# Optimization experiments

Measured on AMD Instinct MI355X. Metric: run time of the kernel, lower is better.

Reference implementation:

```python
import jax, jax.numpy as jnp
import numpy as np

N_NODES = 50000
N_EDGES = 800000
NFEAT = 256
NHID = 128
NCLASS = 40
NLAYERS = 3


def setup_inputs() -> dict:
    key = jax.random.key(0)
    ks = jax.random.split(key, 8)
    x = jax.random.normal(ks[0], (N_NODES, NFEAT), dtype=jnp.float32)
    edge_src = jax.random.randint(ks[1], (N_EDGES,), 0, N_NODES, dtype=jnp.int32)
    edge_dst = jax.random.randint(ks[2], (N_EDGES,), 0, N_NODES, dtype=jnp.int32)
    # Kaiming-ish scaled params
    W_in = jax.random.normal(ks[3], (NFEAT, NHID), dtype=jnp.float32) / np.sqrt(NFEAT)
    b_in = jnp.zeros((NHID,), dtype=jnp.float32)
    W_mlps = jax.random.normal(ks[4], (NLAYERS, NHID, NHID), dtype=jnp.float32) / np.sqrt(NHID)
    b_mlps = jnp.zeros((NLAYERS, NHID), dtype=jnp.float32)
    W_out = jax.random.normal(ks[5], (NHID, NCLASS), dtype=jnp.float32) / np.sqrt(NHID)
    b_out = jnp.zeros((NCLASS,), dtype=jnp.float32)
    return {"x": x, "edge_src": edge_src, "edge_dst": edge_dst,
            "W_in": W_in, "b_in": b_in, "W_mlps": W_mlps, "b_mlps": b_mlps,
            "W_out": W_out, "b_out": b_out}


def reference(x, edge_src, edge_dst, W_in, b_in, W_mlps, b_mlps, W_out, b_out):
    # Dropout is identity in eval mode (training=False).
    n = x.shape[0]
    h = jax.nn.relu(x @ W_in + b_in)                       # [N, H]
    for i in range(NLAYERS):
        # GINConv with eps=0: h' = h + sum_{(s->d) in E} h[s] scattered to d
        agg = jax.ops.segment_sum(h[edge_src], edge_dst, num_segments=n)
        h = jax.nn.relu((h + agg) @ W_mlps[i] + b_mlps[i])  # [N, H]
    logits = h @ W_out + b_out                              # [N, C]
    return jax.nn.log_softmax(logits, axis=1)
```

## Files before the change

kernel.cpp:

```cpp
#include <hip/hip_runtime.h>
#include <math.h>

#define NHID 128
#define NFEAT 256
#define NCLASS 40

typedef __bf16 bf16x8 __attribute__((ext_vector_type(8)));
typedef __bf16 bf16x4 __attribute__((ext_vector_type(4)));
typedef float floatx4 __attribute__((ext_vector_type(4)));


__global__ __launch_bounds__(256) void bucket_hist(const int* __restrict__ edst,
                                                   int* __restrict__ bucket_counts,
                                                   int E, int nbuck) {
    __shared__ int lh[256];
    int tid = threadIdx.x;
    lh[tid] = 0;
    __syncthreads();
    int base = blockIdx.x * 4096;
#pragma unroll
    for (int k = 0; k < 16; ++k) {
        int e = base + k * 256 + tid;
        if (e < E) atomicAdd(&lh[edst[e] >> 8], 1);
    }
    __syncthreads();
    if (tid < nbuck && lh[tid]) atomicAdd(&bucket_counts[tid], lh[tid]);
}

__global__ __launch_bounds__(256) void bucket_scan(const int* __restrict__ counts,
                                                   int* __restrict__ start,
                                                   int* __restrict__ cursor,
                                                   int* __restrict__ row_ptr,
                                                   int nbuck, int E, int N) {
    __shared__ int lds[256];
    int tid = threadIdx.x;
    int v = (tid < nbuck) ? counts[tid] : 0;
    lds[tid] = v;
    __syncthreads();
    for (int off = 1; off < 256; off <<= 1) {
        int t = (tid >= off) ? lds[tid - off] : 0;
        __syncthreads();
        lds[tid] += t;
        __syncthreads();
    }
    int excl = lds[tid] - v;
    if (tid < nbuck) { start[tid] = excl; cursor[tid] = excl; }
    if (tid == 0) { start[nbuck] = E; row_ptr[N] = E; }
}

__global__ __launch_bounds__(256) void bucket_scatter(const int* __restrict__ esrc,
                                                      const int* __restrict__ edst,
                                                      int* __restrict__ cursor,
                                                      unsigned int* __restrict__ bdata,
                                                      int E, int nbuck) {
    __shared__ int lh[256];
    __shared__ int lbase[256];
    int tid = threadIdx.x;
    lh[tid] = 0;
    __syncthreads();
    int base = blockIdx.x * 4096;
    unsigned int recs[16];
    short bks[16];
    short lofs[16];
#pragma unroll
    for (int k = 0; k < 16; ++k) {
        int e = base + k * 256 + tid;
        bks[k] = -1;
        if (e < E) {
            int d = edst[e];
            int s = esrc[e];
            int b = d >> 8;
            recs[k] = ((unsigned int)(d & 255) << 16) | (unsigned int)s;
            bks[k] = (short)b;
            lofs[k] = (short)atomicAdd(&lh[b], 1);
        }
    }
    __syncthreads();
    if (tid < nbuck && lh[tid]) lbase[tid] = atomicAdd(&cursor[tid], lh[tid]);
    __syncthreads();
#pragma unroll
    for (int k = 0; k < 16; ++k) {
        if (bks[k] >= 0) bdata[lbase[bks[k]] + lofs[k]] = recs[k];
    }
}

__global__ __launch_bounds__(256) void bucket_finalize(const unsigned int* __restrict__ bdata,
                                                       const int* __restrict__ start,
                                                       int* __restrict__ row_ptr,
                                                       int* __restrict__ srcs,
                                                       int N) {
    __shared__ int hist[256];
    __shared__ int cur[256];
    int b = blockIdx.x;
    int tid = threadIdx.x;
    int s0 = start[b];
    int cnt = start[b + 1] - s0;
    hist[tid] = 0;
    __syncthreads();
    for (int i = tid; i < cnt; i += 256) atomicAdd(&hist[bdata[s0 + i] >> 16], 1);
    __syncthreads();
    int v0 = hist[tid];
    __syncthreads();
    for (int off = 1; off < 256; off <<= 1) {
        int t = (tid >= off) ? hist[tid - off] : 0;
        __syncthreads();
        hist[tid] += t;
        __syncthreads();
    }
    int excl = hist[tid] - v0;
    cur[tid] = excl;
    int node = b * 256 + tid;
    if (node < N) row_ptr[node] = s0 + excl;
    __syncthreads();
    for (int i = tid; i < cnt; i += 256) {
        unsigned int r = bdata[s0 + i];
        int p = atomicAdd(&cur[r >> 16], 1);
        srcs[s0 + p] = (int)(r & 0xffffu);
    }
}

template <int K>
__global__ __launch_bounds__(256) void transpose_split(const float* __restrict__ src,
                                                       __bf16* __restrict__ dhi,
                                                       __bf16* __restrict__ dlo, int total) {
    int i = blockIdx.x * 256 + threadIdx.x;
    if (i >= total) return;
    int per = 128 * K;
    int l = i / per;
    int r = i - l * per;
    int n = r / K;
    int k = r - n * K;
    float v = src[(size_t)l * per + (size_t)k * 128 + n];
    __bf16 hi = (__bf16)v;
    dhi[i] = hi;
    dlo[i] = (__bf16)(v - (float)hi);
}

__global__ __launch_bounds__(256) void aggregate_fused(const __bf16* __restrict__ hhi,
                                                       const __bf16* __restrict__ hlo,
                                                       const int* __restrict__ row_ptr,
                                                       const int* __restrict__ srcs,
                                                       __bf16* __restrict__ ohi,
                                                       __bf16* __restrict__ olo, int N) {
    int tid = threadIdx.x;
    int node = blockIdx.x * 4 + (tid >> 6);
    if (node >= N) return;
    int lane = tid & 63;
    int g = lane >> 4;
    int c = lane & 15;
    int beg = row_ptr[node];
    int end = row_ptr[node + 1];
    const bf16x8* hv = (const bf16x8*)hhi;

    float a[8], b2[8];
#pragma unroll
    for (int j = 0; j < 8; ++j) { a[j] = 0.f; b2[j] = 0.f; }

    int i = beg;
    for (; i + 8 <= end; i += 8) {
        int s0 = srcs[i + g];
        int s1 = srcs[i + 4 + g];
        bf16x8 v0 = hv[(size_t)s0 * 16 + c];
        bf16x8 v1 = hv[(size_t)s1 * 16 + c];
#pragma unroll
        for (int j = 0; j < 8; ++j) { a[j] += (float)v0[j]; b2[j] += (float)v1[j]; }
    }
    for (; i < end; i += 4) {
        if (i + g < end) {
            int s = srcs[i + g];
            bf16x8 v = hv[(size_t)s * 16 + c];
#pragma unroll
            for (int j = 0; j < 8; ++j) a[j] += (float)v[j];
        }
    }
#pragma unroll
    for (int j = 0; j < 8; ++j) a[j] += b2[j];
#pragma unroll
    for (int j = 0; j < 8; ++j) a[j] += __shfl_xor(a[j], 16);
#pragma unroll
    for (int j = 0; j < 8; ++j) a[j] += __shfl_xor(a[j], 32);

    if (g == 0) {
        bf16x8 sh = ((const bf16x8*)hhi)[(size_t)node * 16 + c];
        bf16x8 sl = ((const bf16x8*)hlo)[(size_t)node * 16 + c];
        bf16x8 whi, wlo;
#pragma unroll
        for (int j = 0; j < 8; ++j) {
            float v = a[j] + (float)sh[j] + (float)sl[j];
            __bf16 h = (__bf16)v;
            whi[j] = h;
            wlo[j] = (__bf16)(v - (float)h);
        }
        ((bf16x8*)ohi)[(size_t)node * 16 + c] = whi;
        ((bf16x8*)olo)[(size_t)node * 16 + c] = wlo;
    }
}

template <int MODE>
__global__ __launch_bounds__(256) void gemm_mfma(
    const float* __restrict__ Af, const __bf16* __restrict__ Ahi,
    const __bf16* __restrict__ Alo,
    const __bf16* __restrict__ Wthi, const __bf16* __restrict__ Wtlo,
    const float* __restrict__ bias, __bf16* __restrict__ Ohi,
    __bf16* __restrict__ Olo, int M, int K) {
    __shared__ __align__(16) char smem[49152];
    __bf16* sAhi = (__bf16*)smem;
    __bf16* sAlo = (__bf16*)(smem + 8192);
    __bf16* sWhi = (__bf16*)(smem + 16384);
    __bf16* sWlo = (__bf16*)(smem + 32768);

    int tid = threadIdx.x;
    int row0 = blockIdx.x * 64;
    int wave = tid >> 6;
    int l = tid & 63;
    int m16 = l & 15;
    int q = l >> 4;
    int axor = m16 & 7;
    int arow = wave * 16 + m16;

    floatx4 acc[8];
#pragma unroll
    for (int t = 0; t < 8; ++t) acc[t] = (floatx4){0.f, 0.f, 0.f, 0.f};

    for (int k0 = 0; k0 < K; k0 += 64) {
#pragma unroll
        for (int it = 0; it < 2; ++it) {
            int lin = it * 2048 + tid * 8;
            int row = lin >> 6, k = lin & 63;
            int g = min(row0 + row, M - 1);
            int off = row * 64 + (((k >> 3) ^ (row & 7)) << 3);
            if (MODE == 0) {
                float4 v0 = *(const float4*)&Af[(size_t)g * K + k0 + k];
                float4 v1 = *(const float4*)&Af[(size_t)g * K + k0 + k + 4];
                float s[8] = {v0.x, v0.y, v0.z, v0.w, v1.x, v1.y, v1.z, v1.w};
                bf16x8 shi, slo;
#pragma unroll
                for (int j = 0; j < 8; ++j) {
                    __bf16 h = (__bf16)s[j];
                    shi[j] = h;
                    slo[j] = (__bf16)(s[j] - (float)h);
                }
                *(bf16x8*)(sAhi + off) = shi;
                *(bf16x8*)(sAlo + off) = slo;
            } else {
                *(bf16x8*)(sAhi + off) = *(const bf16x8*)&Ahi[(size_t)g * 128 + k0 + k];
                *(bf16x8*)(sAlo + off) = *(const bf16x8*)&Alo[(size_t)g * 128 + k0 + k];
            }
        }
#pragma unroll
        for (int it = 0; it < 4; ++it) {
            int lin = it * 2048 + tid * 8;
            int n = lin >> 6, kk = lin & 63;
            int off = n * 64 + (((kk >> 3) ^ (n & 7)) << 3);
            *(bf16x8*)(sWhi + off) = *(const bf16x8*)&Wthi[(size_t)n * K + k0 + kk];
            *(bf16x8*)(sWlo + off) = *(const bf16x8*)&Wtlo[(size_t)n * K + k0 + kk];
        }
        __syncthreads();

#pragma unroll
        for (int s = 0; s < 2; ++s) {
            int sw = (((s * 4 + q) ^ axor) << 3);
            bf16x8 ahi = *(bf16x8*)(sAhi + arow * 64 + sw);
            bf16x8 alo = *(bf16x8*)(sAlo + arow * 64 + sw);
#pragma unroll
            for (int t = 0; t < 8; ++t) {
                int n = t * 16 + m16;
                bf16x8 bhi = *(bf16x8*)(sWhi + n * 64 + sw);
                bf16x8 blo = *(bf16x8*)(sWlo + n * 64 + sw);
                acc[t] = __builtin_amdgcn_mfma_f32_16x16x32_bf16(ahi, bhi, acc[t], 0, 0, 0);
                acc[t] = __builtin_amdgcn_mfma_f32_16x16x32_bf16(alo, bhi, acc[t], 0, 0, 0);
                acc[t] = __builtin_amdgcn_mfma_f32_16x16x32_bf16(ahi, blo, acc[t], 0, 0, 0);
            }
        }
        __syncthreads();
    }

    float* eps = (float*)(smem + 16384);
#pragma unroll
    for (int t = 0; t < 8; ++t) {
        int col = t * 16 + m16;
        float bb = bias[col];
#pragma unroll
        for (int i = 0; i < 4; ++i) {
            int row = wave * 16 + q * 4 + i;
            eps[row * 128 + col] = fmaxf(acc[t][i] + bb, 0.f);
        }
    }
    __syncthreads();
#pragma unroll
    for (int it = 0; it < 8; ++it) {
        int lin = it * 1024 + tid * 4;
        int row = lin >> 7, col = lin & 127;
        int g = row0 + row;
        if (g < M) {
            float4 v = *(float4*)(eps + lin);
            bf16x4 hi, lo;
            float vv[4] = {v.x, v.y, v.z, v.w};
#pragma unroll
            for (int j = 0; j < 4; ++j) {
                __bf16 h = (__bf16)vv[j];
                hi[j] = h;
                lo[j] = (__bf16)(vv[j] - (float)h);
            }
            *(bf16x4*)&Ohi[(size_t)g * 128 + col] = hi;
            *(bf16x4*)&Olo[(size_t)g * 128 + col] = lo;
        }
    }
}

__global__ __launch_bounds__(256) void out_logsoftmax(const __bf16* __restrict__ hhi,
                                                      const __bf16* __restrict__ hlo,
                                                      const float* __restrict__ Wout,
                                                      const float* __restrict__ bout,
                                                      float* __restrict__ out, int M) {
    __shared__ float sW[128 * NCLASS];
    __shared__ float sb[NCLASS];
    __shared__ float sH[32 * 132];
    int tid = threadIdx.x;
    for (int i = tid; i < 128 * NCLASS; i += 256) sW[i] = Wout[i];
    if (tid < NCLASS) sb[tid] = bout[tid];
    int row0 = blockIdx.x * 32;
#pragma unroll
    for (int it = 0; it < 4; ++it) {
        int i = tid * 4 + it * 1024;
        int r = i >> 7, k = i & 127;
        int rr = min(row0 + r, M - 1);
        uint2 uh = *(const uint2*)&hhi[(size_t)rr * 128 + k];
        uint2 ul = *(const uint2*)&hlo[(size_t)rr * 128 + k];
        sH[r * 132 + k + 0] = __uint_as_float(uh.x << 16) + __uint_as_float(ul.x << 16);
        sH[r * 132 + k + 1] = __uint_as_float(uh.x & 0xffff0000u) + __uint_as_float(ul.x & 0xffff0000u);
        sH[r * 132 + k + 2] = __uint_as_float(uh.y << 16) + __uint_as_float(ul.y << 16);
        sH[r * 132 + k + 3] = __uint_as_float(uh.y & 0xffff0000u) + __uint_as_float(ul.y & 0xffff0000u);
    }
    __syncthreads();

    int r = tid >> 3;
    int cg = tid & 7;
    float z[5];
#pragma unroll
    for (int j = 0; j < 5; ++j) z[j] = sb[cg * 5 + j];
    for (int k = 0; k < 128; ++k) {
        float a = sH[r * 132 + k];
#pragma unroll
        for (int j = 0; j < 5; ++j) z[j] += a * sW[k * NCLASS + cg * 5 + j];
    }
    float m = z[0];
#pragma unroll
    for (int j = 1; j < 5; ++j) m = fmaxf(m, z[j]);
    for (int off = 1; off < 8; off <<= 1) m = fmaxf(m, __shfl_xor(m, off));
    float s = 0.f;
#pragma unroll
    for (int j = 0; j < 5; ++j) s += expf(z[j] - m);
    for (int off = 1; off < 8; off <<= 1) s += __shfl_xor(s, off);
    float lse = m + logf(s);
    int row = row0 + r;
    if (row < M) {
#pragma unroll
        for (int j = 0; j < 5; ++j) out[(size_t)row * NCLASS + cg * 5 + j] = z[j] - lse;
    }
}

extern "C" void kernel_launch(void* const* d_in, const int* in_sizes, int n_in,
                              void* d_out, int out_size, void* d_ws, size_t ws_size,
                              hipStream_t stream) {
    const float* x      = (const float*)d_in[0];
    const int*   esrc   = (const int*)d_in[1];
    const int*   edst   = (const int*)d_in[2];
    const float* W_in   = (const float*)d_in[3];
    const float* b_in   = (const float*)d_in[4];
    const float* W_mlps = (const float*)d_in[5];
    const float* b_mlps = (const float*)d_in[6];
    const float* W_out  = (const float*)d_in[7];
    const float* b_out  = (const float*)d_in[8];
    float* out = (float*)d_out;

    int N = in_sizes[0] / NFEAT;
    int E = in_sizes[1];
    int nbuck = (N + 255) >> 8;

    char* ws = (char*)d_ws;
    size_t hb = (((size_t)N * NHID * sizeof(__bf16)) + 255) & ~(size_t)255;
    __bf16* h_hi_a = (__bf16*)ws;
    __bf16* h_lo_a = (__bf16*)(ws + hb);
    __bf16* h_hi_b = (__bf16*)(ws + 2 * hb);
    __bf16* h_lo_b = (__bf16*)(ws + 3 * hb);
    __bf16* sum_hi = (__bf16*)(ws + 4 * hb);
    __bf16* sum_lo = (__bf16*)(ws + 5 * hb);
    unsigned int* bdata = (unsigned int*)(ws + 4 * hb);
    char* ip = ws + 6 * hb;
    int* row_ptr = (int*)ip;  ip += (((size_t)(N + 1) * 4) + 255) & ~(size_t)255;
    int* srcs    = (int*)ip;  ip += (((size_t)E * 4) + 255) & ~(size_t)255;
    int* bucket_counts = (int*)ip;  ip += 1024;
    int* bucket_start  = (int*)ip;  ip += 1024;
    int* bucket_cursor = (int*)ip;  ip += 1024;
    __bf16* Wt_in_hi   = (__bf16*)ip;  ip += 128 * NFEAT * 2;
    __bf16* Wt_in_lo   = (__bf16*)ip;  ip += 128 * NFEAT * 2;
    __bf16* Wt_mlps_hi = (__bf16*)ip;  ip += 3 * 128 * NHID * 2;
    __bf16* Wt_mlps_lo = (__bf16*)ip;  ip += 3 * 128 * NHID * 2;

    int eb4 = (E + 4095) / 4096;

    hipMemsetAsync(bucket_counts, 0, 1024, stream);
    bucket_hist<<<eb4, 256, 0, stream>>>(edst, bucket_counts, E, nbuck);
    bucket_scan<<<1, 256, 0, stream>>>(bucket_counts, bucket_start, bucket_cursor,
                                       row_ptr, nbuck, E, N);
    bucket_scatter<<<eb4, 256, 0, stream>>>(esrc, edst, bucket_cursor, bdata, E, nbuck);
    bucket_finalize<<<nbuck, 256, 0, stream>>>(bdata, bucket_start, row_ptr, srcs, N);

    transpose_split<NFEAT><<<(128 * NFEAT + 255) / 256, 256, 0, stream>>>(
        W_in, Wt_in_hi, Wt_in_lo, 128 * NFEAT);
    transpose_split<NHID><<<(3 * 128 * NHID + 255) / 256, 256, 0, stream>>>(
        W_mlps, Wt_mlps_hi, Wt_mlps_lo, 3 * 128 * NHID);

    int gb = (N + 63) / 64;
    gemm_mfma<0><<<gb, 256, 0, stream>>>(x, (const __bf16*)nullptr, (const __bf16*)nullptr,
                                         Wt_in_hi, Wt_in_lo, b_in, h_hi_a, h_lo_a, N, NFEAT);

    __bf16* cur_hi = h_hi_a; __bf16* cur_lo = h_lo_a;
    __bf16* nxt_hi = h_hi_b; __bf16* nxt_lo = h_lo_b;
    for (int i = 0; i < 3; ++i) {
        aggregate_fused<<<(N + 3) / 4, 256, 0, stream>>>(cur_hi, cur_lo, row_ptr, srcs,
                                                         sum_hi, sum_lo, N);
        gemm_mfma<1><<<gb, 256, 0, stream>>>(
            (const float*)nullptr, sum_hi, sum_lo,
            Wt_mlps_hi + (size_t)i * 128 * NHID, Wt_mlps_lo + (size_t)i * 128 * NHID,
            b_mlps + (size_t)i * NHID, nxt_hi, nxt_lo, N, NHID);
        __bf16* t;
        t = cur_hi; cur_hi = nxt_hi; nxt_hi = t;
        t = cur_lo; cur_lo = nxt_lo; nxt_lo = t;
    }

    out_logsoftmax<<<(N + 31) / 32, 256, 0, stream>>>(cur_hi, cur_lo, W_out, b_out, out, N);
}
```

Baseline: 336.9 us.

## Fuse GIN aggregation with per-layer MLP GEMM and merge weight transposes

Each GIN layer now runs as one kernel: a block of 32 nodes gathers neighbour sums into shared memory as a bf16 hi/lo split, then runs the 128x128 MFMA GEMM with bias and ReLU directly on that tile. The intermediate sum buffers and their global round trip go away, along with one launch per layer. The two weight transpose kernels are merged into one launch. In exchange, weights are read straight from global memory per wave rather than staged in LDS, and each wave gathers 8 nodes serially, which may lower memory-level parallelism in the gather.

Result: slower. 353.9 us (+5.0%).

```diff
diff --git a/kernel.cpp b/kernel.cpp
--- a/kernel.cpp
+++ b/kernel.cpp
@@ -8,7 +8,6 @@
 typedef __bf16 bf16x8 __attribute__((ext_vector_type(8)));
 typedef __bf16 bf16x4 __attribute__((ext_vector_type(4)));
 typedef float floatx4 __attribute__((ext_vector_type(4)));
-
 
 __global__ __launch_bounds__(256) void bucket_hist(const int* __restrict__ edst,
                                                    int* __restrict__ bucket_counts,
@@ -119,87 +118,33 @@
     }
 }
 
-template <int K>
-__global__ __launch_bounds__(256) void transpose_split(const float* __restrict__ src,
-                                                       __bf16* __restrict__ dhi,
-                                                       __bf16* __restrict__ dlo, int total) {
+__global__ __launch_bounds__(256) void transpose_split_all(
+    const float* __restrict__ W_in, const float* __restrict__ W_mlps,
+    __bf16* __restrict__ in_hi, __bf16* __restrict__ in_lo,
+    __bf16* __restrict__ ml_hi, __bf16* __restrict__ ml_lo) {
     int i = blockIdx.x * 256 + threadIdx.x;
-    if (i >= total) return;
-    int per = 128 * K;
-    int l = i / per;
-    int r = i - l * per;
-    int n = r / K;
-    int k = r - n * K;
-    float v = src[(size_t)l * per + (size_t)k * 128 + n];
-    __bf16 hi = (__bf16)v;
-    dhi[i] = hi;
-    dlo[i] = (__bf16)(v - (float)hi);
-}
-
-__global__ __launch_bounds__(256) void aggregate_fused(const __bf16* __restrict__ hhi,
-                                                       const __bf16* __restrict__ hlo,
-                                                       const int* __restrict__ row_ptr,
-                                                       const int* __restrict__ srcs,
-                                                       __bf16* __restrict__ ohi,
-                                                       __bf16* __restrict__ olo, int N) {
-    int tid = threadIdx.x;
-    int node = blockIdx.x * 4 + (tid >> 6);
-    if (node >= N) return;
-    int lane = tid & 63;
-    int g = lane >> 4;
-    int c = lane & 15;
-    int beg = row_ptr[node];
-    int end = row_ptr[node + 1];
-    const bf16x8* hv = (const bf16x8*)hhi;
-
-    float a[8], b2[8];
-#pragma unroll
-    for (int j = 0; j < 8; ++j) { a[j] = 0.f; b2[j] = 0.f; }
-
-    int i = beg;
-    for (; i + 8 <= end; i += 8) {
-        int s0 = srcs[i + g];
-        int s1 = srcs[i + 4 + g];
-        bf16x8 v0 = hv[(size_t)s0 * 16 + c];
-        bf16x8 v1 = hv[(size_t)s1 * 16 + c];
-#pragma unroll
-        for (int j = 0; j < 8; ++j) { a[j] += (float)v0[j]; b2[j] += (float)v1[j]; }
-    }
-    for (; i < end; i += 4) {
-        if (i + g < end) {
-            int s = srcs[i + g];
-            bf16x8 v = hv[(size_t)s * 16 + c];
-#pragma unroll
-            for (int j = 0; j < 8; ++j) a[j] += (float)v[j];
-        }
-    }
-#pragma unroll
-    for (int j = 0; j < 8; ++j) a[j] += b2[j];
-#pragma unroll
-    for (int j = 0; j < 8; ++j) a[j] += __shfl_xor(a[j], 16);
-#pragma unroll
-    for (int j = 0; j < 8; ++j) a[j] += __shfl_xor(a[j], 32);
-
-    if (g == 0) {
-        bf16x8 sh = ((const bf16x8*)hhi)[(size_t)node * 16 + c];
-        bf16x8 sl = ((const bf16x8*)hlo)[(size_t)node * 16 + c];
-        bf16x8 whi, wlo;
-#pragma unroll
-        for (int j = 0; j < 8; ++j) {
-            float v = a[j] + (float)sh[j] + (float)sl[j];
-            __bf16 h = (__bf16)v;
-            whi[j] = h;
-            wlo[j] = (__bf16)(v - (float)h);
-        }
-        ((bf16x8*)ohi)[(size_t)node * 16 + c] = whi;
-        ((bf16x8*)olo)[(size_t)node * 16 + c] = wlo;
-    }
-}
-
-template <int MODE>
-__global__ __launch_bounds__(256) void gemm_mfma(
-    const float* __restrict__ Af, const __bf16* __restrict__ Ahi,
-    const __bf16* __restrict__ Alo,
+    const int total1 = 128 * NFEAT;
+    const int total2 = 3 * 128 * NHID;
+    if (i < total1) {
+        int n = i >> 8, k = i & 255;
+        float v = W_in[(size_t)k * 128 + n];
+        __bf16 hi = (__bf16)v;
+        in_hi[i] = hi;
+        in_lo[i] = (__bf16)(v - (float)hi);
+    } else if (i < total1 + total2) {
+        int j = i - total1;
+        int l = j >> 14;
+        int r = j & 16383;
+        int n = r >> 7, k = r & 127;
+        float v = W_mlps[(size_t)l * 16384 + (size_t)k * 128 + n];
+        __bf16 hi = (__bf16)v;
+        ml_hi[j] = hi;
+        ml_lo[j] = (__bf16)(v - (float)hi);
+    }
+}
+
+__global__ __launch_bounds__(256) void gemm_mfma_in(
+    const float* __restrict__ Af,
     const __bf16* __restrict__ Wthi, const __bf16* __restrict__ Wtlo,
     const float* __restrict__ bias, __bf16* __restrict__ Ohi,
     __bf16* __restrict__ Olo, int M, int K) {
@@ -229,23 +174,18 @@
             int row = lin >> 6, k = lin & 63;
             int g = min(row0 + row, M - 1);
             int off = row * 64 + (((k >> 3) ^ (row & 7)) << 3);
-            if (MODE == 0) {
-                float4 v0 = *(const float4*)&Af[(size_t)g * K + k0 + k];
-                float4 v1 = *(const float4*)&Af[(size_t)g * K + k0 + k + 4];
-                float s[8] = {v0.x, v0.y, v0.z, v0.w, v1.x, v1.y, v1.z, v1.w};
-                bf16x8 shi, slo;
-#pragma unroll
-                for (int j = 0; j < 8; ++j) {
-                    __bf16 h = (__bf16)s[j];
-                    shi[j] = h;
-                    slo[j] = (__bf16)(s[j] - (float)h);
-                }
-                *(bf16x8*)(sAhi + off) = shi;
-                *(bf16x8*)(sAlo + off) = slo;
-            } else {
-                *(bf16x8*)(sAhi + off) = *(const bf16x8*)&Ahi[(size_t)g * 128 + k0 + k];
-                *(bf16x8*)(sAlo + off) = *(const bf16x8*)&Alo[(size_t)g * 128 + k0 + k];
+            float4 v0 = *(const float4*)&Af[(size_t)g * K + k0 + k];
+            float4 v1 = *(const float4*)&Af[(size_t)g * K + k0 + k + 4];
+            float s[8] = {v0.x, v0.y, v0.z, v0.w, v1.x, v1.y, v1.z, v1.w};
+            bf16x8 shi, slo;
+#pragma unroll
+            for (int j = 0; j < 8; ++j) {
+                __bf16 h = (__bf16)s[j];
+                shi[j] = h;
+                slo[j] = (__bf16)(s[j] - (float)h);
             }
+            *(bf16x8*)(sAhi + off) = shi;
+            *(bf16x8*)(sAlo + off) = slo;
         }
 #pragma unroll
         for (int it = 0; it < 4; ++it) {
@@ -304,6 +244,140 @@
             }
             *(bf16x4*)&Ohi[(size_t)g * 128 + col] = hi;
             *(bf16x4*)&Olo[(size_t)g * 128 + col] = lo;
+        }
+    }
+}
+
+__global__ __launch_bounds__(256) void gin_layer_fused(
+    const __bf16* __restrict__ hhi, const __bf16* __restrict__ hlo,
+    const int* __restrict__ row_ptr, const int* __restrict__ srcs,
+    const __bf16* __restrict__ Wthi, const __bf16* __restrict__ Wtlo,
+    const float* __restrict__ bias,
+    __bf16* __restrict__ Ohi, __bf16* __restrict__ Olo, int N) {
+    __shared__ __align__(16) char smem[17408];
+    __bf16* sAhi = (__bf16*)smem;
+    __bf16* sAlo = (__bf16*)(smem + 8192);
+
+    int tid = threadIdx.x;
+    int wave = tid >> 6;
+    int l = tid & 63;
+    int row0 = blockIdx.x * 32;
+
+    int g = l >> 4;
+    int c = l & 15;
+    const bf16x8* hv = (const bf16x8*)hhi;
+    const bf16x8* lv = (const bf16x8*)hlo;
+
+    for (int rr = 0; rr < 8; ++rr) {
+        int row = wave * 8 + rr;
+        int node = min(row0 + row, N - 1);
+        int beg = row_ptr[node];
+        int end = row_ptr[node + 1];
+
+        float a[8], b2[8];
+#pragma unroll
+        for (int j = 0; j < 8; ++j) { a[j] = 0.f; b2[j] = 0.f; }
+
+        int i = beg;
+        for (; i + 8 <= end; i += 8) {
+            int s0 = srcs[i + g];
+            int s1 = srcs[i + 4 + g];
+            bf16x8 v0 = hv[(size_t)s0 * 16 + c];
+            bf16x8 v1 = hv[(size_t)s1 * 16 + c];
+#pragma unroll
+            for (int j = 0; j < 8; ++j) { a[j] += (float)v0[j]; b2[j] += (float)v1[j]; }
+        }
+        for (; i < end; i += 4) {
+            if (i + g < end) {
+                int s = srcs[i + g];
+                bf16x8 v = hv[(size_t)s * 16 + c];
+#pragma unroll
+                for (int j = 0; j < 8; ++j) a[j] += (float)v[j];
+            }
+        }
+#pragma unroll
+        for (int j = 0; j < 8; ++j) a[j] += b2[j];
+#pragma unroll
+        for (int j = 0; j < 8; ++j) a[j] += __shfl_xor(a[j], 16);
+#pragma unroll
+        for (int j = 0; j < 8; ++j) a[j] += __shfl_xor(a[j], 32);
+
+        if (g == 0) {
+            bf16x8 sh = hv[(size_t)node * 16 + c];
+            bf16x8 sl = lv[(size_t)node * 16 + c];
+            bf16x8 whi, wlo;
+#pragma unroll
+            for (int j = 0; j < 8; ++j) {
+                float v = a[j] + (float)sh[j] + (float)sl[j];
+                __bf16 h = (__bf16)v;
+                whi[j] = h;
+                wlo[j] = (__bf16)(v - (float)h);
+            }
+            int off = row * 128 + ((c ^ (row & 7)) << 3);
+            *(bf16x8*)(sAhi + off) = whi;
+            *(bf16x8*)(sAlo + off) = wlo;
+        }
+    }
+    __syncthreads();
+
+    int m16 = l & 15;
+    int q = l >> 4;
+    int mt = wave & 1;
+    int nt0 = (wave >> 1) * 4;
+    int arow = mt * 16 + m16;
+
+    floatx4 acc[4];
+#pragma unroll
+    for (int t = 0; t < 4; ++t) acc[t] = (floatx4){0.f, 0.f, 0.f, 0.f};
+
+#pragma unroll
+    for (int ks = 0; ks < 4; ++ks) {
+        int chunk = ks * 4 + q;
+        int off = arow * 128 + ((chunk ^ (arow & 7)) << 3);
+        bf16x8 ahi = *(bf16x8*)(sAhi + off);
+        bf16x8 alo = *(bf16x8*)(sAlo + off);
+        int kofs = ks * 32 + q * 8;
+#pragma unroll
+        for (int t = 0; t < 4; ++t) {
+            int n = (nt0 + t) * 16 + m16;
+            bf16x8 bhi = *(const bf16x8*)&Wthi[(size_t)n * 128 + kofs];
+            bf16x8 blo = *(const bf16x8*)&Wtlo[(size_t)n * 128 + kofs];
+            acc[t] = __builtin_amdgcn_mfma_f32_16x16x32_bf16(ahi, bhi, acc[t], 0, 0, 0);
+            acc[t] = __builtin_amdgcn_mfma_f32_16x16x32_bf16(alo, bhi, acc[t], 0, 0, 0);
+            acc[t] = __builtin_amdgcn_mfma_f32_16x16x32_bf16(ahi, blo, acc[t], 0, 0, 0);
+        }
+    }
+    __syncthreads();
+
+    float* eps = (float*)smem;
+#pragma unroll
+    for (int t = 0; t < 4; ++t) {
+        int col = (nt0 + t) * 16 + m16;
+        float bb = bias[col];
+#pragma unroll
+        for (int i = 0; i < 4; ++i) {
+            int row = mt * 16 + q * 4 + i;
+            eps[row * 132 + col] = fmaxf(acc[t][i] + bb, 0.f);
+        }
+    }
+    __syncthreads();
+#pragma unroll
+    for (int it = 0; it < 4; ++it) {
+        int lin = it * 1024 + tid * 4;
+        int row = lin >> 7, col = lin & 127;
+        int gg = row0 + row;
+        if (gg < N) {
+            float4 v = *(float4*)(eps + row * 132 + col);
+            bf16x4 hi, lo;
+            float vv[4] = {v.x, v.y, v.z, v.w};
+#pragma unroll
+            for (int j = 0; j < 4; ++j) {
+                __bf16 h = (__bf16)vv[j];
+                hi[j] = h;
+                lo[j] = (__bf16)(vv[j] - (float)h);
+            }
+            *(bf16x4*)&Ohi[(size_t)gg * 128 + col] = hi;
+            *(bf16x4*)&Olo[(size_t)gg * 128 + col] = lo;
         }
     }
 }
@@ -384,10 +458,8 @@
     __bf16* h_lo_a = (__bf16*)(ws + hb);
     __bf16* h_hi_b = (__bf16*)(ws + 2 * hb);
     __bf16* h_lo_b = (__bf16*)(ws + 3 * hb);
-    __bf16* sum_hi = (__bf16*)(ws + 4 * hb);
-    __bf16* sum_lo = (__bf16*)(ws + 5 * hb);
-    unsigned int* bdata = (unsigned int*)(ws + 4 * hb);
-    char* ip = ws + 6 * hb;
+    unsigned int* bdata = (unsigned int*)(ws + 2 * hb);
+    char* ip = ws + 4 * hb;
     int* row_ptr = (int*)ip;  ip += (((size_t)(N + 1) * 4) + 255) & ~(size_t)255;
     int* srcs    = (int*)ip;  ip += (((size_t)E * 4) + 255) & ~(size_t)255;
     int* bucket_counts = (int*)ip;  ip += 1024;
@@ -407,24 +479,20 @@
     bucket_scatter<<<eb4, 256, 0, stream>>>(esrc, edst, bucket_cursor, bdata, E, nbuck);
     bucket_finalize<<<nbuck, 256, 0, stream>>>(bdata, bucket_start, row_ptr, srcs, N);
 
-    transpose_split<NFEAT><<<(128 * NFEAT + 255) / 256, 256, 0, stream>>>(
-        W_in, Wt_in_hi, Wt_in_lo, 128 * NFEAT);
-    transpose_split<NHID><<<(3 * 128 * NHID + 255) / 256, 256, 0, stream>>>(
-        W_mlps, Wt_mlps_hi, Wt_mlps_lo, 3 * 128 * NHID);
-
-    int gb = (N + 63) / 64;
-    gemm_mfma<0><<<gb, 256, 0, stream>>>(x, (const __bf16*)nullptr, (const __bf16*)nullptr,
-                                         Wt_in_hi, Wt_in_lo, b_in, h_hi_a, h_lo_a, N, NFEAT);
+    transpose_split_all<<<320, 256, 0, stream>>>(W_in, W_mlps, Wt_in_hi, Wt_in_lo,
+                                                 Wt_mlps_hi, Wt_mlps_lo);
+
+    gemm_mfma_in<<<(N + 63) / 64, 256, 0, stream>>>(x, Wt_in_hi, Wt_in_lo, b_in,
+                                                    h_hi_a, h_lo_a, N, NFEAT);
 
     __bf16* cur_hi = h_hi_a; __bf16* cur_lo = h_lo_a;
     __bf16* nxt_hi = h_hi_b; __bf16* nxt_lo = h_lo_b;
+    int fb = (N + 31) / 32;
     for (int i = 0; i < 3; ++i) {
-        aggregate_fused<<<(N + 3) / 4, 256, 0, stream>>>(cur_hi, cur_lo, row_ptr, srcs,
-                                                         sum_hi, sum_lo, N);
-        gemm_mfma<1><<<gb, 256, 0, stream>>>(
-            (const float*)nullptr, sum_hi, sum_lo,
+        gin_layer_fused<<<fb, 256, 0, stream>>>(
+            cur_hi, cur_lo, row_ptr, srcs,
             Wt_mlps_hi + (size_t)i * 128 * NHID, Wt_mlps_lo + (size_t)i * 128 * NHID,
-            b_mlps + (size_t)i * NHID, nxt_hi, nxt_lo, N, NHID);
+            b_mlps + (size_t)i * NHID, nxt_hi, nxt_lo, N);
         __bf16* t;
         t = cur_hi; cur_hi = nxt_hi; nxt_hi = t;
         t = cur_lo; cur_lo = nxt_lo; nxt_lo = t;
```

## Split aggregation into feature-quarter blocks and merge weight transposes

Applied to the files above, without the earlier changes.

The aggregation kernel now splits the 128 feature columns into four quarters, each handled by a separate set of blocks. Each quarter-block covers 16 nodes, with 4 lanes per node per edge slot. The launch order puts all blocks for one quarter together, so the gathered working set per wave of blocks is a quarter of the feature table. This should improve L2 hit rates on random neighbor gathers, at the cost of reading row_ptr and srcs four times and launching four times as many blocks. The two weight transpose/split kernels are also merged into one launch.

New measurement: 359.3 us. +6.6%, slower.

```diff
diff --git a/kernel.cpp b/kernel.cpp
--- a/kernel.cpp
+++ b/kernel.cpp
@@ -8,7 +8,6 @@
 typedef __bf16 bf16x8 __attribute__((ext_vector_type(8)));
 typedef __bf16 bf16x4 __attribute__((ext_vector_type(4)));
 typedef float floatx4 __attribute__((ext_vector_type(4)));
-
 
 __global__ __launch_bounds__(256) void bucket_hist(const int* __restrict__ edst,
                                                    int* __restrict__ bucket_counts,
@@ -119,70 +118,80 @@
     }
 }
 
-template <int K>
-__global__ __launch_bounds__(256) void transpose_split(const float* __restrict__ src,
-                                                       __bf16* __restrict__ dhi,
-                                                       __bf16* __restrict__ dlo, int total) {
+__global__ __launch_bounds__(256) void transpose_split_all(
+    const float* __restrict__ W_in, const float* __restrict__ W_mlps,
+    __bf16* __restrict__ in_hi, __bf16* __restrict__ in_lo,
+    __bf16* __restrict__ ml_hi, __bf16* __restrict__ ml_lo) {
     int i = blockIdx.x * 256 + threadIdx.x;
-    if (i >= total) return;
-    int per = 128 * K;
-    int l = i / per;
-    int r = i - l * per;
-    int n = r / K;
-    int k = r - n * K;
-    float v = src[(size_t)l * per + (size_t)k * 128 + n];
-    __bf16 hi = (__bf16)v;
-    dhi[i] = hi;
-    dlo[i] = (__bf16)(v - (float)hi);
-}
-
-__global__ __launch_bounds__(256) void aggregate_fused(const __bf16* __restrict__ hhi,
-                                                       const __bf16* __restrict__ hlo,
-                                                       const int* __restrict__ row_ptr,
-                                                       const int* __restrict__ srcs,
-                                                       __bf16* __restrict__ ohi,
-                                                       __bf16* __restrict__ olo, int N) {
-    int tid = threadIdx.x;
-    int node = blockIdx.x * 4 + (tid >> 6);
-    if (node >= N) return;
-    int lane = tid & 63;
-    int g = lane >> 4;
-    int c = lane & 15;
+    const int total1 = 128 * NFEAT;
+    const int total2 = 3 * 128 * NHID;
+    if (i < total1) {
+        int n = i >> 8, k = i & 255;
+        float v = W_in[(size_t)k * 128 + n];
+        __bf16 hi = (__bf16)v;
+        in_hi[i] = hi;
+        in_lo[i] = (__bf16)(v - (float)hi);
+    } else if (i < total1 + total2) {
+        int j = i - total1;
+        int l = j >> 14;
+        int r = j & 16383;
+        int n = r >> 7, k = r & 127;
+        float v = W_mlps[(size_t)l * 16384 + (size_t)k * 128 + n];
+        __bf16 hi = (__bf16)v;
+        ml_hi[j] = hi;
+        ml_lo[j] = (__bf16)(v - (float)hi);
+    }
+}
+
+__global__ __launch_bounds__(256) void aggregate_q(
+    const __bf16* __restrict__ hhi, const __bf16* __restrict__ hlo,
+    const int* __restrict__ row_ptr, const int* __restrict__ srcs,
+    __bf16* __restrict__ ohi, __bf16* __restrict__ olo, int N, int ntiles) {
+    int bq = blockIdx.x / ntiles;
+    int tile = blockIdx.x - bq * ntiles;
+    int tid = threadIdx.x;
+    int wave = tid >> 6;
+    int l = tid & 63;
+    int sub = l >> 4;
+    int slot = (l >> 2) & 3;
+    int c = l & 3;
+    int node0 = tile * 16 + wave * 4 + sub;
+    int node = min(node0, N - 1);
+    int qo = bq * 4 + c;
     int beg = row_ptr[node];
     int end = row_ptr[node + 1];
     const bf16x8* hv = (const bf16x8*)hhi;
+    const bf16x8* lv = (const bf16x8*)hlo;
 
     float a[8], b2[8];
 #pragma unroll
     for (int j = 0; j < 8; ++j) { a[j] = 0.f; b2[j] = 0.f; }
 
-    int i = beg;
-    for (; i + 8 <= end; i += 8) {
-        int s0 = srcs[i + g];
-        int s1 = srcs[i + 4 + g];
-        bf16x8 v0 = hv[(size_t)s0 * 16 + c];
-        bf16x8 v1 = hv[(size_t)s1 * 16 + c];
+    int i = beg + slot;
+    for (; i + 4 < end; i += 8) {
+        int s0 = srcs[i];
+        int s1 = srcs[i + 4];
+        bf16x8 v0 = hv[(size_t)s0 * 16 + qo];
+        bf16x8 v1 = hv[(size_t)s1 * 16 + qo];
 #pragma unroll
         for (int j = 0; j < 8; ++j) { a[j] += (float)v0[j]; b2[j] += (float)v1[j]; }
     }
-    for (; i < end; i += 4) {
-        if (i + g < end) {
-            int s = srcs[i + g];
-            bf16x8 v = hv[(size_t)s * 16 + c];
-#pragma unroll
-            for (int j = 0; j < 8; ++j) a[j] += (float)v[j];
-        }
+    if (i < end) {
+        int s0 = srcs[i];
+        bf16x8 v0 = hv[(size_t)s0 * 16 + qo];
+#pragma unroll
+        for (int j = 0; j < 8; ++j) a[j] += (float)v0[j];
     }
 #pragma unroll
     for (int j = 0; j < 8; ++j) a[j] += b2[j];
 #pragma unroll
-    for (int j = 0; j < 8; ++j) a[j] += __shfl_xor(a[j], 16);
-#pragma unroll
-    for (int j = 0; j < 8; ++j) a[j] += __shfl_xor(a[j], 32);
-
-    if (g == 0) {
-        bf16x8 sh = ((const bf16x8*)hhi)[(size_t)node * 16 + c];
-        bf16x8 sl = ((const bf16x8*)hlo)[(size_t)node * 16 + c];
+    for (int j = 0; j < 8; ++j) a[j] += __shfl_xor(a[j], 4);
+#pragma unroll
+    for (int j = 0; j < 8; ++j) a[j] += __shfl_xor(a[j], 8);
+
+    if (slot == 0 && node0 < N) {
+        bf16x8 sh = hv[(size_t)node * 16 + qo];
+        bf16x8 sl = lv[(size_t)node * 16 + qo];
         bf16x8 whi, wlo;
 #pragma unroll
         for (int j = 0; j < 8; ++j) {
@@ -191,8 +200,8 @@
             whi[j] = h;
             wlo[j] = (__bf16)(v - (float)h);
         }
-        ((bf16x8*)ohi)[(size_t)node * 16 + c] = whi;
-        ((bf16x8*)olo)[(size_t)node * 16 + c] = wlo;
+        ((bf16x8*)ohi)[(size_t)node * 16 + qo] = whi;
+        ((bf16x8*)olo)[(size_t)node * 16 + qo] = wlo;
     }
 }
 
@@ -400,28 +409,27 @@
 
     int eb4 = (E + 4095) / 4096;
 
-    hipMemsetAsync(bucket_counts, 0, 1024, stream);
+    (void)hipMemsetAsync(bucket_counts, 0, 1024, stream);
     bucket_hist<<<eb4, 256, 0, stream>>>(edst, bucket_counts, E, nbuck);
     bucket_scan<<<1, 256, 0, stream>>>(bucket_counts, bucket_start, bucket_cursor,
                                        row_ptr, nbuck, E, N);
     bucket_scatter<<<eb4, 256, 0, stream>>>(esrc, edst, bucket_cursor, bdata, E, nbuck);
     bucket_finalize<<<nbuck, 256, 0, stream>>>(bdata, bucket_start, row_ptr, srcs, N);
 
-    transpose_split<NFEAT><<<(128 * NFEAT + 255) / 256, 256, 0, stream>>>(
-        W_in, Wt_in_hi, Wt_in_lo, 128 * NFEAT);
-    transpose_split<NHID><<<(3 * 128 * NHID + 255) / 256, 256, 0, stream>>>(
-        W_mlps, Wt_mlps_hi, Wt_mlps_lo, 3 * 128 * NHID);
-
-    int gb = (N + 63) / 64;
-    gemm_mfma<0><<<gb, 256, 0, stream>>>(x, (const __bf16*)nullptr, (const __bf16*)nullptr,
-                                         Wt_in_hi, Wt_in_lo, b_in, h_hi_a, h_lo_a, N, NFEAT);
+    transpose_split_all<<<320, 256, 0, stream>>>(W_in, W_mlps, Wt_in_hi, Wt_in_lo,
+                                                 Wt_mlps_hi, Wt_mlps_lo);
+
+    gemm_mfma<0><<<(N + 63) / 64, 256, 0, stream>>>(
+        x, (const __bf16*)nullptr, (const __bf16*)nullptr,
+        Wt_in_hi, Wt_in_lo, b_in, h_hi_a, h_lo_a, N, NFEAT);
 
     __bf16* cur_hi = h_hi_a; __bf16* cur_lo = h_lo_a;
     __bf16* nxt_hi = h_hi_b; __bf16* nxt_lo = h_lo_b;
+    int ntiles = (N + 15) / 16;
     for (int i = 0; i < 3; ++i) {
-        aggregate_fused<<<(N + 3) / 4, 256, 0, stream>>>(cur_hi, cur_lo, row_ptr, srcs,
-                                                         sum_hi, sum_lo, N);
-        gemm_mfma<1><<<gb, 256, 0, stream>>>(
+        aggregate_q<<<4 * ntiles, 256, 0, stream>>>(cur_hi, cur_lo, row_ptr, srcs,
+                                                    sum_hi, sum_lo, N, ntiles);
+        gemm_mfma<1><<<(N + 63) / 64, 256, 0, stream>>>(
             (const float*)nullptr, sum_hi, sum_lo,
             Wt_mlps_hi + (size_t)i * 128 * NHID, Wt_mlps_lo + (size_t)i * 128 * NHID,
             b_mlps + (size_t)i * NHID, nxt_hi, nxt_lo, N, NHID);
```

## Fuse weight transposes into scatter, drop memset, unroll aggregation to four accumulators

Applied to the files above, without the earlier changes.

The bucket histogram now writes per-block partial histograms that the scan kernel sums, which removes the memset and the global atomics. The two weight transpose/split kernels are folded into extra blocks of the bucket_scatter launch, cutting two kernel launches. The aggregation loop is unrolled to 16 edges per iteration with four independent accumulators, putting more gathers in flight. The scan now does a serial loop over about 196 partial rows per thread, and the unroll raises register pressure in the aggregation kernel.

Result: slower. 357.1 us (+6.0%).

```diff
diff --git a/kernel.cpp b/kernel.cpp
--- a/kernel.cpp
+++ b/kernel.cpp
@@ -9,10 +9,9 @@
 typedef __bf16 bf16x4 __attribute__((ext_vector_type(4)));
 typedef float floatx4 __attribute__((ext_vector_type(4)));
 
-
 __global__ __launch_bounds__(256) void bucket_hist(const int* __restrict__ edst,
-                                                   int* __restrict__ bucket_counts,
-                                                   int E, int nbuck) {
+                                                   int* __restrict__ part_hist,
+                                                   int E) {
     __shared__ int lh[256];
     int tid = threadIdx.x;
     lh[tid] = 0;
@@ -24,17 +23,19 @@
         if (e < E) atomicAdd(&lh[edst[e] >> 8], 1);
     }
     __syncthreads();
-    if (tid < nbuck && lh[tid]) atomicAdd(&bucket_counts[tid], lh[tid]);
-}
-
-__global__ __launch_bounds__(256) void bucket_scan(const int* __restrict__ counts,
+    part_hist[blockIdx.x * 256 + tid] = lh[tid];
+}
+
+__global__ __launch_bounds__(256) void bucket_scan(const int* __restrict__ part_hist,
+                                                   int nblk,
                                                    int* __restrict__ start,
                                                    int* __restrict__ cursor,
                                                    int* __restrict__ row_ptr,
                                                    int nbuck, int E, int N) {
     __shared__ int lds[256];
     int tid = threadIdx.x;
-    int v = (tid < nbuck) ? counts[tid] : 0;
+    int v = 0;
+    for (int b = 0; b < nblk; ++b) v += part_hist[b * 256 + tid];
     lds[tid] = v;
     __syncthreads();
     for (int off = 1; off < 256; off <<= 1) {
@@ -52,10 +53,38 @@
                                                       const int* __restrict__ edst,
                                                       int* __restrict__ cursor,
                                                       unsigned int* __restrict__ bdata,
-                                                      int E, int nbuck) {
+                                                      int E, int nbuck, int eb4,
+                                                      const float* __restrict__ W_in,
+                                                      const float* __restrict__ W_mlps,
+                                                      __bf16* __restrict__ in_hi,
+                                                      __bf16* __restrict__ in_lo,
+                                                      __bf16* __restrict__ ml_hi,
+                                                      __bf16* __restrict__ ml_lo) {
+    int tid = threadIdx.x;
+    if (blockIdx.x >= eb4) {
+        int i = (blockIdx.x - eb4) * 256 + tid;
+        const int total1 = 128 * NFEAT;
+        const int total2 = 3 * 128 * NHID;
+        if (i < total1) {
+            int n = i >> 8, k = i & 255;
+            float v = W_in[(size_t)k * 128 + n];
+            __bf16 hi = (__bf16)v;
+            in_hi[i] = hi;
+            in_lo[i] = (__bf16)(v - (float)hi);
+        } else if (i < total1 + total2) {
+            int j = i - total1;
+            int l = j >> 14;
+            int r = j & 16383;
+            int n = r >> 7, k = r & 127;
+            float v = W_mlps[(size_t)l * 16384 + (size_t)k * 128 + n];
+            __bf16 hi = (__bf16)v;
+            ml_hi[j] = hi;
+            ml_lo[j] = (__bf16)(v - (float)hi);
+        }
+        return;
+    }
     __shared__ int lh[256];
     __shared__ int lbase[256];
-    int tid = threadIdx.x;
     lh[tid] = 0;
     __syncthreads();
     int base = blockIdx.x * 4096;
@@ -119,23 +148,6 @@
     }
 }
 
-template <int K>
-__global__ __launch_bounds__(256) void transpose_split(const float* __restrict__ src,
-                                                       __bf16* __restrict__ dhi,
-                                                       __bf16* __restrict__ dlo, int total) {
-    int i = blockIdx.x * 256 + threadIdx.x;
-    if (i >= total) return;
-    int per = 128 * K;
-    int l = i / per;
-    int r = i - l * per;
-    int n = r / K;
-    int k = r - n * K;
-    float v = src[(size_t)l * per + (size_t)k * 128 + n];
-    __bf16 hi = (__bf16)v;
-    dhi[i] = hi;
-    dlo[i] = (__bf16)(v - (float)hi);
-}
-
 __global__ __launch_bounds__(256) void aggregate_fused(const __bf16* __restrict__ hhi,
                                                        const __bf16* __restrict__ hlo,
                                                        const int* __restrict__ row_ptr,
@@ -145,48 +157,70 @@
     int tid = threadIdx.x;
     int node = blockIdx.x * 4 + (tid >> 6);
     if (node >= N) return;
-    int lane = tid & 63;
-    int g = lane >> 4;
-    int c = lane & 15;
+    int l = tid & 63;
+    int g = l >> 4;
+    int c = l & 15;
     int beg = row_ptr[node];
     int end = row_ptr[node + 1];
     const bf16x8* hv = (const bf16x8*)hhi;
-
-    float a[8], b2[8];
-#pragma unroll
-    for (int j = 0; j < 8; ++j) { a[j] = 0.f; b2[j] = 0.f; }
+    const bf16x8* lv = (const bf16x8*)hlo;
+
+    float a0[8], a1[8], a2[8], a3[8];
+#pragma unroll
+    for (int j = 0; j < 8; ++j) { a0[j] = 0.f; a1[j] = 0.f; a2[j] = 0.f; a3[j] = 0.f; }
 
     int i = beg;
-    for (; i + 8 <= end; i += 8) {
+    for (; i + 16 <= end; i += 16) {
+        int s0 = srcs[i + g];
+        int s1 = srcs[i + 4 + g];
+        int s2 = srcs[i + 8 + g];
+        int s3 = srcs[i + 12 + g];
+        bf16x8 v0 = hv[(size_t)s0 * 16 + c];
+        bf16x8 v1 = hv[(size_t)s1 * 16 + c];
+        bf16x8 v2 = hv[(size_t)s2 * 16 + c];
+        bf16x8 v3 = hv[(size_t)s3 * 16 + c];
+#pragma unroll
+        for (int j = 0; j < 8; ++j) {
+            a0[j] += (float)v0[j];
+            a1[j] += (float)v1[j];
+            a2[j] += (float)v2[j];
+            a3[j] += (float)v3[j];
+        }
+    }
+    if (i + 8 <= end) {
         int s0 = srcs[i + g];
         int s1 = srcs[i + 4 + g];
         bf16x8 v0 = hv[(size_t)s0 * 16 + c];
         bf16x8 v1 = hv[(size_t)s1 * 16 + c];
 #pragma unroll
-        for (int j = 0; j < 8; ++j) { a[j] += (float)v0[j]; b2[j] += (float)v1[j]; }
+        for (int j = 0; j < 8; ++j) {
+            a0[j] += (float)v0[j];
+            a1[j] += (float)v1[j];
+        }
+        i += 8;
     }
     for (; i < end; i += 4) {
         if (i + g < end) {
             int s = srcs[i + g];
             bf16x8 v = hv[(size_t)s * 16 + c];
 #pragma unroll
-            for (int j = 0; j < 8; ++j) a[j] += (float)v[j];
-        }
-    }
-#pragma unroll
-    for (int j = 0; j < 8; ++j) a[j] += b2[j];
-#pragma unroll
-    for (int j = 0; j < 8; ++j) a[j] += __shfl_xor(a[j], 16);
-#pragma unroll
-    for (int j = 0; j < 8; ++j) a[j] += __shfl_xor(a[j], 32);
+            for (int j = 0; j < 8; ++j) a0[j] += (float)v[j];
+        }
+    }
+#pragma unroll
+    for (int j = 0; j < 8; ++j) a0[j] += (a1[j] + a2[j]) + a3[j];
+#pragma unroll
+    for (int j = 0; j < 8; ++j) a0[j] += __shfl_xor(a0[j], 16);
+#pragma unroll
+    for (int j = 0; j < 8; ++j) a0[j] += __shfl_xor(a0[j], 32);
 
     if (g == 0) {
-        bf16x8 sh = ((const bf16x8*)hhi)[(size_t)node * 16 + c];
-        bf16x8 sl = ((const bf16x8*)hlo)[(size_t)node * 16 + c];
+        bf16x8 sh = hv[(size_t)node * 16 + c];
+        bf16x8 sl = lv[(size_t)node * 16 + c];
         bf16x8 whi, wlo;
 #pragma unroll
         for (int j = 0; j < 8; ++j) {
-            float v = a[j] + (float)sh[j] + (float)sl[j];
+            float v = a0[j] + (float)sh[j] + (float)sl[j];
             __bf16 h = (__bf16)v;
             whi[j] = h;
             wlo[j] = (__bf16)(v - (float)h);
@@ -377,6 +411,7 @@
     int N = in_sizes[0] / NFEAT;
     int E = in_sizes[1];
     int nbuck = (N + 255) >> 8;
+    int eb4 = (E + 4095) / 4096;
 
     char* ws = (char*)d_ws;
     size_t hb = (((size_t)N * NHID * sizeof(__bf16)) + 255) & ~(size_t)255;
@@ -390,7 +425,7 @@
     char* ip = ws + 6 * hb;
     int* row_ptr = (int*)ip;  ip += (((size_t)(N + 1) * 4) + 255) & ~(size_t)255;
     int* srcs    = (int*)ip;  ip += (((size_t)E * 4) + 255) & ~(size_t)255;
-    int* bucket_counts = (int*)ip;  ip += 1024;
+    int* part_hist     = (int*)ip;  ip += 256 * 256 * 4;
     int* bucket_start  = (int*)ip;  ip += 1024;
     int* bucket_cursor = (int*)ip;  ip += 1024;
     __bf16* Wt_in_hi   = (__bf16*)ip;  ip += 128 * NFEAT * 2;
@@ -398,30 +433,25 @@
     __bf16* Wt_mlps_hi = (__bf16*)ip;  ip += 3 * 128 * NHID * 2;
     __bf16* Wt_mlps_lo = (__bf16*)ip;  ip += 3 * 128 * NHID * 2;
 
-    int eb4 = (E + 4095) / 4096;
-
-    hipMemsetAsync(bucket_counts, 0, 1024, stream);
-    bucket_hist<<<eb4, 256, 0, stream>>>(edst, bucket_counts, E, nbuck);
-    bucket_scan<<<1, 256, 0, stream>>>(bucket_counts, bucket_start, bucket_cursor,
+    bucket_hist<<<eb4, 256, 0, stream>>>(edst, part_hist, E);
+    bucket_scan<<<1, 256, 0, stream>>>(part_hist, eb4, bucket_start, bucket_cursor,
                                        row_ptr, nbuck, E, N);
-    bucket_scatter<<<eb4, 256, 0, stream>>>(esrc, edst, bucket_cursor, bdata, E, nbuck);
+    bucket_scatter<<<eb4 + 320, 256, 0, stream>>>(esrc, edst, bucket_cursor, bdata,
+                                                  E, nbuck, eb4, W_in, W_mlps,
+                                                  Wt_in_hi, Wt_in_lo,
+                                                  Wt_mlps_hi, Wt_mlps_lo);
     bucket_finalize<<<nbuck, 256, 0, stream>>>(bdata, bucket_start, row_ptr, srcs, N);
 
-    transpose_split<NFEAT><<<(128 * NFEAT + 255) / 256, 256, 0, stream>>>(
-        W_in, Wt_in_hi, Wt_in_lo, 128 * NFEAT);
-    transpose_split<NHID><<<(3 * 128 * NHID + 255) / 256, 256, 0, stream>>>(
-        W_mlps, Wt_mlps_hi, Wt_mlps_lo, 3 * 128 * NHID);
-
-    int gb = (N + 63) / 64;
-    gemm_mfma<0><<<gb, 256, 0, stream>>>(x, (const __bf16*)nullptr, (const __bf16*)nullptr,
-                                         Wt_in_hi, Wt_in_lo, b_in, h_hi_a, h_lo_a, N, NFEAT);
+    gemm_mfma<0><<<(N + 63) / 64, 256, 0, stream>>>(
+        x, (const __bf16*)nullptr, (const __bf16*)nullptr,
+        Wt_in_hi, Wt_in_lo, b_in, h_hi_a, h_lo_a, N, NFEAT);
 
     __bf16* cur_hi = h_hi_a; __bf16* cur_lo = h_lo_a;
     __bf16* nxt_hi = h_hi_b; __bf16* nxt_lo = h_lo_b;
     for (int i = 0; i < 3; ++i) {
         aggregate_fused<<<(N + 3) / 4, 256, 0, stream>>>(cur_hi, cur_lo, row_ptr, srcs,
                                                          sum_hi, sum_lo, N);
-        gemm_mfma<1><<<gb, 256, 0, stream>>>(
+        gemm_mfma<1><<<(N + 63) / 64, 256, 0, stream>>>(
             (const float*)nullptr, sum_hi, sum_lo,
             Wt_mlps_hi + (size_t)i * 128 * NHID, Wt_mlps_lo + (size_t)i * 128 * NHID,
             b_mlps + (size_t)i * NHID, nxt_hi, nxt_lo, N, NHID);
```
